# Optimization experiments

Measured on AMD Instinct MI355X. Metric: run time of the kernel, lower is better.

## Reference

```python
import jax, jax.numpy as jnp
import numpy as np

B, N, K, D = 8, 4096, 16, 256


def layer_norm(x, g, b, eps=1e-5):
    m = jnp.mean(x, axis=-1, keepdims=True)
    v = jnp.var(x, axis=-1, keepdims=True)
    return (x - m) * jax.lax.rsqrt(v + eps) * g + b


def setup_inputs() -> dict:
    key = jax.random.key(0)
    ks = jax.random.split(key, 8)

    def lin(k, fi, fo):
        return (jax.random.normal(k, (fi, fo), jnp.float32) / np.sqrt(fi).astype(np.float32),
                jnp.zeros((fo,), jnp.float32))

    coordinates = jax.random.normal(ks[0], (B, N, 3), jnp.float32)
    W1, b1 = lin(ks[1], 10, D // 4)
    W2, b2 = lin(ks[2], D // 4, D // 2)
    W3, b3 = lin(ks[3], D // 2, D)
    Wa1, ba1 = lin(ks[4], D, D)
    Wa2, ba2 = lin(ks[5], D, D)
    return {
        'coordinates': coordinates,
        'W1': W1, 'b1': b1, 'g1': jnp.ones((D // 4,)), 'be1': jnp.zeros((D // 4,)),
        'W2': W2, 'b2': b2, 'g2': jnp.ones((D // 2,)), 'be2': jnp.zeros((D // 2,)),
        'W3': W3, 'b3': b3, 'g3': jnp.ones((D,)), 'be3': jnp.zeros((D,)),
        'Wa1': Wa1, 'ba1': ba1, 'ga1': jnp.ones((D,)), 'bea1': jnp.zeros((D,)),
        'Wa2': Wa2, 'ba2': ba2,
    }


def reference(coordinates, W1, b1, g1, be1, W2, b2, g2, be2, W3, b3, g3, be3,
              Wa1, ba1, ga1, bea1, Wa2, ba2):
    # kNN via squared-distance matrix (monotone in Euclidean distance)
    sq = jnp.sum(coordinates * coordinates, axis=-1)  # [B,N]
    d2 = sq[:, :, None] + sq[:, None, :] - 2.0 * jnp.einsum('bnd,bmd->bnm', coordinates, coordinates)
    _, idx = jax.lax.top_k(-d2, K)  # smallest K distances, [B,N,K]

    nbr = jax.vmap(lambda c, i: c[i])(coordinates, idx)  # [B,N,K,3]
    rel = nbr - coordinates[:, :, None, :]               # relative positions
    dist = jnp.linalg.norm(rel, axis=-1, keepdims=True)  # [B,N,K,1]
    rn = rel / (dist + 1e-6)
    axy = jnp.arctan2(rn[..., 1], rn[..., 0])[..., None]
    axz = jnp.arctan2(rn[..., 2], rn[..., 0])[..., None]
    ayz = jnp.arctan2(rn[..., 2], rn[..., 1])[..., None]
    geom = jnp.concatenate([dist, rel, axy, axz, ayz, rn], axis=-1)  # [B,N,K,10]

    # encoder MLP
    h = jax.nn.relu(layer_norm(geom @ W1 + b1, g1, be1))
    h = jax.nn.relu(layer_norm(h @ W2 + b2, g2, be2))
    h = layer_norm(h @ W3 + b3, g3, be3)

    agg = jnp.mean(h, axis=2)  # mean over neighbors -> [B,N,D]

    # aggregator MLP
    out = jax.nn.relu(layer_norm(agg @ Wa1 + ba1, ga1, bea1)) @ Wa2 + ba2
    return out
```

## Files before the change

kernel.cpp:

```cpp
#include <hip/hip_runtime.h>
#include <hip/hip_bf16.h>
#include <math.h>

#define BB 8
#define NN 4096
#define KK 16
#define DD 256

typedef __hip_bfloat16 bf16;
typedef _Float16 half8 __attribute__((ext_vector_type(8)));
typedef float f32x4 __attribute__((ext_vector_type(4)));

union HFU { _Float16 h; unsigned short u; };
__device__ __forceinline__ unsigned short f2h(float x) { HFU v; v.h = (_Float16)x; return v.u; }

#define CONV_TOTAL 273344
#define O_COORD 0
#define O_W1 98304
#define O_b1 98944
#define O_g1 99008
#define O_be1 99072
#define O_W2 99136
#define O_b2 107328
#define O_g2 107456
#define O_be2 107584
#define O_W3 107712
#define O_b3 140480
#define O_g3 140736
#define O_be3 140992
#define O_Wa1 141248
#define O_ba1 206784
#define O_ga1 207040
#define O_bea1 207296
#define O_Wa2 207552
#define O_ba2 273088

#define F_W1 0
#define F_W2 2048
#define F_W3 10240
#define F_A1 43008
#define F_A2 108544
#define FRAG_TOTAL 174080

struct SrcPtrs {
  const void* p[19];
};

__global__ __launch_bounds__(256) void convert_kernel(SrcPtrs sp, float* __restrict__ dst) {
  static constexpr int OFF[20] = {
      0,      98304,  98944,  99008,  99072,  99136,  107328, 107456, 107584,
      107712, 140480, 140736, 140992, 141248, 206784, 207040, 207296, 207552,
      273088, 273344};
  const int i = blockIdx.x * 256 + threadIdx.x;
  if (i >= CONV_TOTAL) return;
  const unsigned tag = ((const unsigned*)sp.p[3])[0];
  const bool isb = (tag == 0x3F803F80u);
  int s = 0;
#pragma unroll
  for (int j = 1; j < 19; j++)
    if (i >= OFF[j]) s = j;
  const int local = i - OFF[s];
  float v = isb ? __bfloat162float(((const bf16*)sp.p[s])[local])
                : ((const float*)sp.p[s])[local];
  dst[i] = v;
}

__global__ __launch_bounds__(256) void swizzle_kernel(const float* __restrict__ conv,
                                                      unsigned short* __restrict__ frag) {
  const int t = blockIdx.x * 256 + threadIdx.x;
  if (t >= FRAG_TOTAL) return;
  int l, e;
  if (t < 2048) { l = 0; e = t; }
  else if (t < 10240) { l = 1; e = t - 2048; }
  else if (t < 43008) { l = 2; e = t - 10240; }
  else if (t < 108544) { l = 3; e = t - 43008; }
  else { l = 4; e = t - 108544; }
  static constexpr int WOFF[5] = {O_W1, O_W2, O_W3, O_Wa1, O_Wa2};
  static constexpr int NDIM[5] = {64, 128, 256, 256, 256};
  static constexpr int NTC[5] = {4, 8, 16, 16, 16};
  static constexpr int KREAL[5] = {10, 64, 128, 256, 256};
  static constexpr int HOFF[5] = {F_W1, F_W2, F_W3, F_A1, F_A2};
  const int j = e & 7;
  const int lane = (e >> 3) & 63;
  const int tile = e >> 9;
  const int nt = tile % NTC[l];
  const int kt = tile / NTC[l];
  const int k = kt * 32 + (lane >> 4) * 8 + j;
  const int n = nt * 16 + (lane & 15);
  float w = (k < KREAL[l]) ? conv[WOFF[l] + k * NDIM[l] + n] : 0.0f;
  frag[HOFF[l] + e] = f2h(w);
}

__device__ __forceinline__ float sq3_rn(float x, float y, float z) {
  return __fadd_rn(__fadd_rn(__fmul_rn(x, x), __fmul_rn(y, y)), __fmul_rn(z, z));
}
__device__ __forceinline__ float dot3_rn(float ax, float ay, float az, float bx, float by, float bz) {
  return __fadd_rn(__fadd_rn(__fmul_rn(ax, bx), __fmul_rn(ay, by)), __fmul_rn(az, bz));
}
__device__ __forceinline__ unsigned f2ord(float f) {
  unsigned u = __float_as_uint(f);
  return (u & 0x80000000u) ? ~u : (u | 0x80000000u);
}
__device__ __forceinline__ float ord2f(unsigned o) {
  unsigned u = (o & 0x80000000u) ? (o & 0x7FFFFFFFu) : ~o;
  return __uint_as_float(u);
}

__device__ __forceinline__ unsigned long long bitonic64(unsigned long long key, int lane) {
#pragma unroll
  for (int k = 2; k <= 64; k <<= 1) {
#pragma unroll
    for (int jj = k >> 1; jj > 0; jj >>= 1) {
      unsigned long long v = __shfl_xor(key, jj, 64);
      bool asc = ((lane & k) == 0);
      bool up = ((lane & jj) != 0);
      unsigned long long mn = (key < v) ? key : v;
      unsigned long long mx2 = (key < v) ? v : key;
      key = (up == asc) ? mx2 : mn;
    }
  }
  return key;
}

__global__ __launch_bounds__(512) void cellsort_kernel(const float* __restrict__ conv,
                                                       float4* __restrict__ sorted,
                                                       int* __restrict__ sidx) {
  __shared__ unsigned hist[512];
  __shared__ unsigned scanb[512];
  const int b = blockIdx.x;
  const int tid = threadIdx.x;
  const float* cb = conv + O_COORD + (size_t)b * NN * 3;
  hist[tid] = 0;
  __syncthreads();
  float xs[8], ys[8], zs[8];
  int cell[8];
  unsigned rank[8];
#pragma unroll
  for (int u = 0; u < 8; u++) {
    int p = u * 512 + tid;
    float x = cb[p * 3 + 0], y = cb[p * 3 + 1], z = cb[p * 3 + 2];
    xs[u] = x; ys[u] = y; zs[u] = z;
    int ix = min(7, max(0, (int)floorf(x + 4.0f)));
    int iy = min(7, max(0, (int)floorf(y + 4.0f)));
    int iz = min(7, max(0, (int)floorf(z + 4.0f)));
    int m = ((ix & 1) | ((ix & 2) << 2) | ((ix & 4) << 4)) |
            (((iy & 1) | ((iy & 2) << 2) | ((iy & 4) << 4)) << 1) |
            (((iz & 1) | ((iz & 2) << 2) | ((iz & 4) << 4)) << 2);
    cell[u] = m;
    rank[u] = atomicAdd(&hist[m], 1u);
  }
  __syncthreads();
  scanb[tid] = hist[tid];
  __syncthreads();
  for (int off = 1; off < 512; off <<= 1) {
    unsigned t = (tid >= off) ? scanb[tid - off] : 0u;
    __syncthreads();
    scanb[tid] += t;
    __syncthreads();
  }
#pragma unroll
  for (int u = 0; u < 8; u++) {
    unsigned base = scanb[cell[u]] - hist[cell[u]];
    unsigned pos = base + rank[u];
    sorted[(size_t)b * NN + pos] =
        make_float4(xs[u], ys[u], zs[u], sq3_rn(xs[u], ys[u], zs[u]));
    sidx[(size_t)b * NN + pos] = u * 512 + tid;
  }
}

__global__ __launch_bounds__(256) void knn_wave_kernel(const float4* __restrict__ soa,
                                                       const int* __restrict__ sI,
                                                       int* __restrict__ idx_out) {
  const int lane = threadIdx.x & 63;
  const int wid = blockIdx.x * 4 + (threadIdx.x >> 6);
  const int q0 = wid * 4;
  const int b = q0 >> 12;
  const float4* P = soa + (size_t)b * NN;
  const int* I = sI + (size_t)b * NN;
  const int qr = q0 & (NN - 1);
  const int base = qr >> 6;

  float cx[4], cy[4], cz[4], sqn[4];
  int qix[4];
#pragma unroll
  for (int j = 0; j < 4; j++) {
    float4 c = P[qr + j];
    cx[j] = c.x; cy[j] = c.y; cz[j] = c.z; sqn[j] = c.w;
    qix[j] = I[qr + j];
  }

  unsigned long long R[4], pend[4];
  float tauf[4];
  int A[4] = {0, 0, 0, 0};
#pragma unroll
  for (int j = 0; j < 4; j++) pend[j] = ~0ull;

  auto MERGE = [&](int j) {
    unsigned long long key =
        (lane < 16) ? R[j] : ((lane < 16 + A[j]) ? pend[j] : ~0ull);
    key = bitonic64(key, lane);
    R[j] = key;
    tauf[j] = ord2f((unsigned)(unsigned long long)__builtin_amdgcn_readlane(
        (int)(unsigned)(key >> 32), 15));
    A[j] = 0;
  };

  auto APPEND = [&](int j, unsigned long long msk, int cc, unsigned long long key) {
    unsigned rank = __builtin_amdgcn_mbcnt_hi(
        (unsigned)(msk >> 32), __builtin_amdgcn_mbcnt_lo((unsigned)msk, 0u));
    const bool flag = ((msk >> lane) & 1ull) != 0;
    const int lim = 16 + A[j];
    const int nf = lane - (int)rank;
    const int dst = flag ? (lim + (int)rank) : (nf < lim ? nf : nf + cc);
    int src = __builtin_amdgcn_ds_permute(dst << 2, lane) & 63;
    unsigned lo = (unsigned)__builtin_amdgcn_ds_bpermute(src << 2, (int)(unsigned)key);
    unsigned hi = (unsigned)__builtin_amdgcn_ds_bpermute(src << 2, (int)(unsigned)(key >> 32));
    const bool cons = (lane >= lim) && (lane < lim + cc);
    if (cons) pend[j] = (((unsigned long long)hi) << 32) | lo;
    A[j] += cc;
  };

  const int b0 = base * 64 + lane;
  float4 f0 = P[b0];
  int i0 = I[b0];
  const int b1 = ((base + 1) & 63) * 64 + lane;
  float4 f1 = P[b1];
  int i1 = I[b1];
  const int b2i = ((base + 2) & 63) * 64 + lane;
  float4 f2 = P[b2i];
  int i2 = I[b2i];

#pragma unroll
  for (int j = 0; j < 4; j++) {
    float dot = dot3_rn(cx[j], cy[j], cz[j], f0.x, f0.y, f0.z);
    float d2 = __fsub_rn(__fadd_rn(sqn[j], f0.w), __fmul_rn(2.0f, dot));
    unsigned long long key =
        (((unsigned long long)f2ord(d2)) << 32) | (unsigned)i0;
    key = bitonic64(key, lane);
    R[j] = key;
    tauf[j] = ord2f((unsigned)(unsigned long long)__builtin_amdgcn_readlane(
        (int)(unsigned)(key >> 32), 15));
  }

  for (int t = 1; t < 64; t++) {
    const float4 c = f1;
    const int iv = i1;
    f1 = f2; i1 = i2;
    if (t + 2 < 64) {
      const int nb = ((base + t + 2) & 63) * 64 + lane;
      f2 = P[nb];
      i2 = I[nb];
    }
    float d2v[4];
    unsigned long long pm[4];
#pragma unroll
    for (int j = 0; j < 4; j++) {
      float dot = dot3_rn(cx[j], cy[j], cz[j], c.x, c.y, c.z);
      d2v[j] = __fsub_rn(__fadd_rn(sqn[j], c.w), __fmul_rn(2.0f, dot));
      pm[j] = __ballot(d2v[j] <= tauf[j]);
    }
    if (!(pm[0] | pm[1] | pm[2] | pm[3])) continue;
#pragma unroll
    for (int j = 0; j < 4; j++) {
      unsigned long long rem = pm[j];
      if (!rem) continue;
      const unsigned long long key =
          (((unsigned long long)f2ord(d2v[j])) << 32) | (unsigned)iv;
      int cc = __builtin_popcountll(rem);
      while (A[j] + cc > 48) {
        if (A[j] == 0) {
          unsigned long long take = rem & 0xFFFFFFFFull;
          APPEND(j, take, __builtin_popcountll(take), key);
          rem ^= take;
        }
        MERGE(j);
        rem &= __ballot(d2v[j] <= tauf[j]);
        cc = __builtin_popcountll(rem);
      }
      if (cc) APPEND(j, rem, cc, key);
    }
  }

#pragma unroll
  for (int j = 0; j < 4; j++) {
    if (A[j]) MERGE(j);
    if (lane < KK)
      idx_out[((size_t)b * NN + (unsigned)qix[j]) * KK + lane] =
          (int)(R[j] & 0xFFFFFFFFull);
  }
}

template <int KT>
__device__ __forceinline__ void load_afrags(half8* A, const unsigned short* lF,
                                            int rowe, int lane) {
#pragma unroll
  for (int kt = 0; kt < KT; kt++) {
    int off = (lane & 15) * rowe + kt * 32 + (lane >> 4) * 8;
    A[kt] = *reinterpret_cast<const half8*>(lF + off);
  }
}

template <int NT>
__device__ __forceinline__ void init_acc(f32x4* acc, const float* __restrict__ bias,
                                         int lane) {
  const int col = lane & 15;
#pragma unroll
  for (int nt = 0; nt < NT; nt++) {
    float bv = bias[nt * 16 + col];
    acc[nt] = {bv, bv, bv, bv};
  }
}

template <int KT, int NT>
__device__ __forceinline__ void gemm_acc(f32x4* acc, const half8* A,
                                         const unsigned short* bb, int lane) {
#pragma unroll
  for (int kt = 0; kt < KT; kt++)
#pragma unroll
    for (int nt = 0; nt < NT; nt++) {
      const half8 bf = *reinterpret_cast<const half8*>(bb + (kt * NT + nt) * 512 + lane * 8);
      acc[nt] = __builtin_amdgcn_mfma_f32_16x16x32_f16(A[kt], bf, acc[nt], 0, 0, 0);
    }
}

template <int NT>
__device__ __forceinline__ void ln_stats(const f32x4* acc, float* m, float* rs) {
  float s[4] = {0.f, 0.f, 0.f, 0.f}, s2[4] = {0.f, 0.f, 0.f, 0.f};
#pragma unroll
  for (int nt = 0; nt < NT; nt++)
#pragma unroll
    for (int r = 0; r < 4; r++) {
      float v = acc[nt][r];
      s[r] += v;
      s2[r] += v * v;
    }
#pragma unroll
  for (int msk = 1; msk <= 8; msk <<= 1)
#pragma unroll
    for (int r = 0; r < 4; r++) {
      s[r] += __shfl_xor(s[r], msk, 64);
      s2[r] += __shfl_xor(s2[r], msk, 64);
    }
  const float invN = 1.0f / (NT * 16);
#pragma unroll
  for (int r = 0; r < 4; r++) {
    m[r] = s[r] * invN;
    float var = s2[r] * invN - m[r] * m[r];
    rs[r] = rsqrtf(var + 1e-5f);
  }
}

template <int NT, bool RELU>
__device__ __forceinline__ void ln_store(const f32x4* acc, const float* m, const float* rs,
                                         const float* __restrict__ g, const float* __restrict__ be,
                                         unsigned short* lF, int rowe, int lane) {
  const int col = lane & 15;
  const int rbase = (lane >> 4) * 4;
#pragma unroll
  for (int nt = 0; nt < NT; nt++) {
    float gv = g[nt * 16 + col], bv = be[nt * 16 + col];
#pragma unroll
    for (int r = 0; r < 4; r++) {
      float v = (acc[nt][r] - m[r]) * rs[r] * gv + bv;
      if (RELU) v = fmaxf(v, 0.0f);
      lF[(rbase + r) * rowe + nt * 16 + col] = f2h(v);
    }
  }
}

__device__ __forceinline__ void stage_b(unsigned short* bbuf,
                                        const unsigned short* __restrict__ src,
                                        int n_u4, int tid) {
  const uint4* s = reinterpret_cast<const uint4*>(src);
  uint4* d = reinterpret_cast<uint4*>(bbuf);
  for (int i = tid; i < n_u4; i += 256) d[i] = s[i];
}

#define ROWE_E 136
#define PSTR_E (16 * ROWE_E)

__global__ __launch_bounds__(256, 3) void encoder_mfma(
    const float* __restrict__ conv, const int* __restrict__ nbr,
    const unsigned short* __restrict__ frag, unsigned short* __restrict__ agF) {
  __shared__ unsigned short planes[4 * PSTR_E];
  __shared__ unsigned short Bbuf[10240];
  const int tid = threadIdx.x;
  const int lane = tid & 63;
  const int wave = tid >> 6;
  const int point = blockIdx.x * 4 + wave;
  const int b = point >> 12;
  const int n = point & (NN - 1);
  const float* cb = conv + O_COORD + (size_t)b * NN * 3;
  unsigned short* lF = planes + wave * PSTR_E;
  const int g = lane >> 4;
  const int col = lane & 15;

  {
    int pl = tid >> 6, row = (tid >> 2) & 15, part = tid & 3;
    *reinterpret_cast<uint4*>(planes + pl * PSTR_E + row * ROWE_E + part * 8) =
        make_uint4(0u, 0u, 0u, 0u);
    stage_b(Bbuf, frag + F_W1, 1280, tid);
  }
  __syncthreads();

  if (lane < 16) {
    float cxq = cb[n * 3 + 0], cyq = cb[n * 3 + 1], czq = cb[n * 3 + 2];
    int id = nbr[(size_t)point * KK + lane];
    float rx = __fsub_rn(cb[id * 3 + 0], cxq);
    float ry = __fsub_rn(cb[id * 3 + 1], cyq);
    float rz = __fsub_rn(cb[id * 3 + 2], czq);
    float dist = __fsqrt_rn(sq3_rn(rx, ry, rz));
    float den = __fadd_rn(dist, 1e-6f);
    float ux = __fdiv_rn(rx, den), uy = __fdiv_rn(ry, den), uz = __fdiv_rn(rz, den);
    float ge[10];
    ge[0] = dist; ge[1] = rx; ge[2] = ry; ge[3] = rz;
    ge[4] = atan2f(uy, ux); ge[5] = atan2f(uz, ux); ge[6] = atan2f(uz, uy);
    ge[7] = ux; ge[8] = uy; ge[9] = uz;
#pragma unroll
    for (int c = 0; c < 10; c++) lF[lane * ROWE_E + c] = f2h(ge[c]);
  }

  {
    half8 x0;
    load_afrags<1>(&x0, lF, ROWE_E, lane);
    f32x4 a1[4];
#pragma unroll
    for (int m = 0; m < 4; m++) {
      const float4 bv = *reinterpret_cast<const float4*>(conv + O_b1 + m * 16 + g * 4);
      a1[m] = {bv.x, bv.y, bv.z, bv.w};
      const half8 wf = *reinterpret_cast<const half8*>(Bbuf + m * 512 + lane * 8);
      a1[m] = __builtin_amdgcn_mfma_f32_16x16x32_f16(wf, x0, a1[m], 0, 0, 0);
    }
    float s = 0.f, s2 = 0.f;
#pragma unroll
    for (int m = 0; m < 4; m++)
#pragma unroll
      for (int r = 0; r < 4; r++) { float v = a1[m][r]; s += v; s2 += v * v; }
    s += __shfl_xor(s, 16, 64); s += __shfl_xor(s, 32, 64);
    s2 += __shfl_xor(s2, 16, 64); s2 += __shfl_xor(s2, 32, 64);
    const float mu = s * (1.0f / 64.0f);
    const float rsg = rsqrtf(s2 * (1.0f / 64.0f) - mu * mu + 1e-5f);
#pragma unroll
    for (int m = 0; m < 4; m++) {
      const float4 gv = *reinterpret_cast<const float4*>(conv + O_g1 + m * 16 + g * 4);
      const float4 bev = *reinterpret_cast<const float4*>(conv + O_be1 + m * 16 + g * 4);
      unsigned long long pk = 0;
#pragma unroll
      for (int r = 0; r < 4; r++) {
        float v = fmaxf((a1[m][r] - mu) * rsg * (&gv.x)[r] + (&bev.x)[r], 0.0f);
        pk |= ((unsigned long long)f2h(v)) << (16 * r);
      }
      *reinterpret_cast<unsigned long long*>(lF + col * ROWE_E + m * 16 + g * 4) = pk;
    }
  }

  {
    half8 x2[2];
    load_afrags<2>(x2, lF, ROWE_E, lane);
    f32x4 a2[8];
#pragma unroll
    for (int m = 0; m < 8; m++) {
      const float4 bv = *reinterpret_cast<const float4*>(conv + O_b2 + m * 16 + g * 4);
      a2[m] = {bv.x, bv.y, bv.z, bv.w};
    }
#pragma unroll
    for (int kt = 0; kt < 2; kt++)
#pragma unroll
      for (int m = 0; m < 8; m++) {
        const half8 wf =
            *reinterpret_cast<const half8*>(Bbuf + 2048 + (kt * 8 + m) * 512 + lane * 8);
        a2[m] = __builtin_amdgcn_mfma_f32_16x16x32_f16(wf, x2[kt], a2[m], 0, 0, 0);
      }
    float s = 0.f, s2 = 0.f;
#pragma unroll
    for (int m = 0; m < 8; m++)
#pragma unroll
      for (int r = 0; r < 4; r++) { float v = a2[m][r]; s += v; s2 += v * v; }
    s += __shfl_xor(s, 16, 64); s += __shfl_xor(s, 32, 64);
    s2 += __shfl_xor(s2, 16, 64); s2 += __shfl_xor(s2, 32, 64);
    const float mu = s * (1.0f / 128.0f);
    const float rsg = rsqrtf(s2 * (1.0f / 128.0f) - mu * mu + 1e-5f);
#pragma unroll
    for (int m = 0; m < 8; m++) {
      const float4 gv = *reinterpret_cast<const float4*>(conv + O_g2 + m * 16 + g * 4);
      const float4 bev = *reinterpret_cast<const float4*>(conv + O_be2 + m * 16 + g * 4);
      unsigned long long pk = 0;
#pragma unroll
      for (int r = 0; r < 4; r++) {
        float v = fmaxf((a2[m][r] - mu) * rsg * (&gv.x)[r] + (&bev.x)[r], 0.0f);
        pk |= ((unsigned long long)f2h(v)) << (16 * r);
      }
      *reinterpret_cast<unsigned long long*>(lF + col * ROWE_E + m * 16 + g * 4) = pk;
    }
  }

  half8 A3[4];
  load_afrags<4>(A3, lF, ROWE_E, lane);
  f32x4 acc[16];
  init_acc<16>(acc, conv + O_b3, lane);
  {
    const unsigned short* W3 = frag + F_W3;
#pragma unroll
    for (int kt = 0; kt < 4; kt++)
#pragma unroll
      for (int nt = 0; nt < 16; nt++) {
        const half8 bf =
            *reinterpret_cast<const half8*>(W3 + (kt * 16 + nt) * 512 + lane * 8);
        acc[nt] = __builtin_amdgcn_mfma_f32_16x16x32_f16(A3[kt], bf, acc[nt], 0, 0, 0);
      }
  }

  {
    float m[4], rs[4];
    ln_stats<16>(acc, m, rs);
    float sv[16];
#pragma unroll
    for (int nt = 0; nt < 16; nt++) {
      float gvv = conv[O_g3 + nt * 16 + col], bvv = conv[O_be3 + nt * 16 + col];
      float s = 0.f;
#pragma unroll
      for (int r = 0; r < 4; r++) s += (acc[nt][r] - m[r]) * rs[r] * gvv + bvv;
      s += __shfl_xor(s, 16, 64);
      s += __shfl_xor(s, 32, 64);
      sv[nt] = s * (1.0f / 16.0f);
    }
    if (lane < 16) {
      size_t base = (size_t)point * DD;
#pragma unroll
      for (int nt = 0; nt < 16; nt++) agF[base + nt * 16 + lane] = f2h(sv[nt]);
    }
  }
}

#define ROWE_A 264

__global__ __launch_bounds__(256) void aggmlp_mfma(
    const float* __restrict__ conv, const unsigned short* __restrict__ agF,
    const unsigned short* __restrict__ a1, const unsigned short* __restrict__ a2,
    const unsigned* __restrict__ g1raw, void* __restrict__ out) {
  __shared__ unsigned short lds[4][16 * ROWE_A];
  const int lane = threadIdx.x & 63;
  const int wave = threadIdx.x >> 6;
  const int row0 = (blockIdx.x * 4 + wave) * 16;
  unsigned short* lF = lds[wave];

#pragma unroll
  for (int t = 0; t < 8; t++) {
    int v = t * 64 + lane;
    int row = v >> 5;
    int c0 = (v & 31) * 8;
    *reinterpret_cast<uint4*>(lF + row * ROWE_A + c0) =
        *reinterpret_cast<const uint4*>(agF + ((size_t)(row0 + row) * DD + c0));
  }
  __syncthreads();

  float m[4], rs[4];
  f32x4 acc[16];
  {
    half8 A[8];
    load_afrags<8>(A, lF, ROWE_A, lane);
    init_acc<16>(acc, conv + O_ba1, lane);
    gemm_acc<8, 16>(acc, A, a1, lane);
    ln_stats<16>(acc, m, rs);
    ln_store<16, true>(acc, m, rs, conv + O_ga1, conv + O_bea1, lF, ROWE_A, lane);
  }
  __syncthreads();
  {
    half8 A[8];
    load_afrags<8>(A, lF, ROWE_A, lane);
    init_acc<16>(acc, conv + O_ba2, lane);
    gemm_acc<8, 16>(acc, A, a2, lane);
  }
  const bool isb = (g1raw[0] == 0x3F803F80u);
  const int col = lane & 15;
  const int rbase = (lane >> 4) * 4;
  if (isb) {
    bf16* o = (bf16*)out;
#pragma unroll
    for (int nt = 0; nt < 16; nt++)
#pragma unroll
      for (int r = 0; r < 4; r++)
        o[(size_t)(row0 + rbase + r) * DD + nt * 16 + col] = __float2bfloat16(acc[nt][r]);
  } else {
    float* o = (float*)out;
#pragma unroll
    for (int nt = 0; nt < 16; nt++)
#pragma unroll
      for (int r = 0; r < 4; r++)
        o[(size_t)(row0 + rbase + r) * DD + nt * 16 + col] = acc[nt][r];
  }
}

extern "C" void kernel_launch(void* const* d_in, const int* in_sizes, int n_in,
                              void* d_out, int out_size, void* d_ws, size_t ws_size,
                              hipStream_t stream) {
  char* ws = (char*)d_ws;
  float* conv = (float*)ws;
  int* idx_ws = (int*)(ws + 1093376);
  unsigned short* agF = (unsigned short*)(ws + 3190528);
  unsigned short* frag = (unsigned short*)(ws + 19967744);
  float4* sorted = (float4*)(ws + 20315904);
  int* sidx = (int*)(ws + 20840192);

  SrcPtrs sp;
  for (int i = 0; i < 19; i++) sp.p[i] = d_in[i];

  convert_kernel<<<(CONV_TOTAL + 255) / 256, 256, 0, stream>>>(sp, conv);
  swizzle_kernel<<<(FRAG_TOTAL + 255) / 256, 256, 0, stream>>>(conv, frag);
  cellsort_kernel<<<BB, 512, 0, stream>>>(conv, sorted, sidx);

  knn_wave_kernel<<<BB * NN / 16, 256, 0, stream>>>(sorted, sidx, idx_ws);

  encoder_mfma<<<BB * NN / 4, 256, 0, stream>>>(conv, idx_ws, frag, agF);

  aggmlp_mfma<<<BB * NN / 64, 256, 0, stream>>>(conv, agF, frag + F_A1, frag + F_A2,
                                                (const unsigned*)d_in[3], d_out);
}
```

Baseline: 384.5 us.

## Prune kNN candidate blocks using per-block bounding boxes

Adds a kernel that computes an axis-aligned bounding box for each 64-point block of cell-sorted coordinates. The kNN kernel then computes a lower-bound distance from its 4 queries to each block and visits only blocks whose bound is within the current worst top-K threshold plus a margin, rechecking the bound as the threshold tightens. This is meant to skip most of the 64-block brute-force scan per wave. It adds a small extra launch and a data-dependent loop with irregular loads. The margin is a safety fudge, and pruning with squared distances from fp32-rounded keys could in rare cases drop true neighbors.

```diff
diff --git a/kernel.cpp b/kernel.cpp
--- a/kernel.cpp
+++ b/kernel.cpp
@@ -41,6 +41,8 @@
 #define F_A1 43008
 #define F_A2 108544
 #define FRAG_TOTAL 174080
+
+#define PRUNE_MARGIN 0.0625f
 
 struct SrcPtrs {
   const void* p[19];
@@ -168,8 +170,33 @@
   }
 }
 
+__global__ __launch_bounds__(256) void bbox_kernel(const float4* __restrict__ sorted,
+                                                   float4* __restrict__ bbmn,
+                                                   float4* __restrict__ bbmx) {
+  const int lane = threadIdx.x & 63;
+  const int gid = blockIdx.x * 4 + (threadIdx.x >> 6);
+  float4 p = sorted[(size_t)gid * 64 + lane];
+  float mnx = p.x, mny = p.y, mnz = p.z;
+  float mxx = p.x, mxy = p.y, mxz = p.z;
+#pragma unroll
+  for (int d = 1; d < 64; d <<= 1) {
+    mnx = fminf(mnx, __shfl_xor(mnx, d, 64));
+    mny = fminf(mny, __shfl_xor(mny, d, 64));
+    mnz = fminf(mnz, __shfl_xor(mnz, d, 64));
+    mxx = fmaxf(mxx, __shfl_xor(mxx, d, 64));
+    mxy = fmaxf(mxy, __shfl_xor(mxy, d, 64));
+    mxz = fmaxf(mxz, __shfl_xor(mxz, d, 64));
+  }
+  if (lane == 0) {
+    bbmn[gid] = make_float4(mnx, mny, mnz, 0.0f);
+    bbmx[gid] = make_float4(mxx, mxy, mxz, 0.0f);
+  }
+}
+
 __global__ __launch_bounds__(256) void knn_wave_kernel(const float4* __restrict__ soa,
                                                        const int* __restrict__ sI,
+                                                       const float4* __restrict__ bbmn,
+                                                       const float4* __restrict__ bbmx,
                                                        int* __restrict__ idx_out) {
   const int lane = threadIdx.x & 63;
   const int wid = blockIdx.x * 4 + (threadIdx.x >> 6);
@@ -188,6 +215,23 @@
     cx[j] = c.x; cy[j] = c.y; cz[j] = c.z; sqn[j] = c.w;
     qix[j] = I[qr + j];
   }
+
+  float4 bmn = bbmn[b * 64 + lane];
+  float4 bmx = bbmx[b * 64 + lane];
+  float4 f0 = P[base * 64 + lane];
+  int i0 = I[base * 64 + lane];
+
+  float qnx = fminf(fminf(cx[0], cx[1]), fminf(cx[2], cx[3]));
+  float qxx = fmaxf(fmaxf(cx[0], cx[1]), fmaxf(cx[2], cx[3]));
+  float qny = fminf(fminf(cy[0], cy[1]), fminf(cy[2], cy[3]));
+  float qxy = fmaxf(fmaxf(cy[0], cy[1]), fmaxf(cy[2], cy[3]));
+  float qnz = fminf(fminf(cz[0], cz[1]), fminf(cz[2], cz[3]));
+  float qxz = fmaxf(fmaxf(cz[0], cz[1]), fmaxf(cz[2], cz[3]));
+
+  float dx = fmaxf(fmaxf(bmn.x - qxx, qnx - bmx.x), 0.0f);
+  float dy = fmaxf(fmaxf(bmn.y - qxy, qny - bmx.y), 0.0f);
+  float dz = fmaxf(fmaxf(bmn.z - qxz, qnz - bmx.z), 0.0f);
+  const float lb = dx * dx + dy * dy + dz * dz;
 
   unsigned long long R[4], pend[4];
   float tauf[4];
@@ -220,16 +264,6 @@
     A[j] += cc;
   };
 
-  const int b0 = base * 64 + lane;
-  float4 f0 = P[b0];
-  int i0 = I[b0];
-  const int b1 = ((base + 1) & 63) * 64 + lane;
-  float4 f1 = P[b1];
-  int i1 = I[b1];
-  const int b2i = ((base + 2) & 63) * 64 + lane;
-  float4 f2 = P[b2i];
-  int i2 = I[b2i];
-
 #pragma unroll
   for (int j = 0; j < 4; j++) {
     float dot = dot3_rn(cx[j], cy[j], cz[j], f0.x, f0.y, f0.z);
@@ -242,14 +276,34 @@
         (int)(unsigned)(key >> 32), 15));
   }
 
-  for (int t = 1; t < 64; t++) {
-    const float4 c = f1;
-    const int iv = i1;
-    f1 = f2; i1 = i2;
-    if (t + 2 < 64) {
-      const int nb = ((base + t + 2) & 63) * 64 + lane;
-      f2 = P[nb];
-      i2 = I[nb];
+  float tmax = fmaxf(fmaxf(tauf[0], tauf[1]), fmaxf(tauf[2], tauf[3]));
+  unsigned long long mask =
+      __ballot(lb <= tmax + PRUNE_MARGIN) & ~(1ull << base);
+  const int ro = (base + 1) & 63;
+  auto rot = [&](unsigned long long m) {
+    return ro ? ((m >> ro) | (m << (64 - ro))) : m;
+  };
+  unsigned long long rm = rot(mask);
+
+  int tA = -1, tB = -1, iA = 0, iB = 0;
+  float4 fA, fB;
+  if (rm) {
+    int tz = __builtin_ctzll(rm); rm &= rm - 1;
+    tA = (ro + tz) & 63; fA = P[tA * 64 + lane]; iA = I[tA * 64 + lane];
+  }
+  if (rm) {
+    int tz = __builtin_ctzll(rm); rm &= rm - 1;
+    tB = (ro + tz) & 63; fB = P[tB * 64 + lane]; iB = I[tB * 64 + lane];
+  }
+  while (tA >= 0) {
+    const float4 c = fA;
+    const int iv = iA;
+    tA = tB; fA = fB; iA = iB;
+    if (rm) {
+      int tz = __builtin_ctzll(rm); rm &= rm - 1;
+      tB = (ro + tz) & 63; fB = P[tB * 64 + lane]; iB = I[tB * 64 + lane];
+    } else {
+      tB = -1;
     }
     float d2v[4];
     unsigned long long pm[4];
@@ -279,6 +333,8 @@
       }
       if (cc) APPEND(j, rem, cc, key);
     }
+    tmax = fmaxf(fmaxf(tauf[0], tauf[1]), fmaxf(tauf[2], tauf[3]));
+    rm &= rot(__ballot(lb <= tmax + PRUNE_MARGIN));
   }
 
 #pragma unroll
@@ -601,6 +657,8 @@
   unsigned short* frag = (unsigned short*)(ws + 19967744);
   float4* sorted = (float4*)(ws + 20315904);
   int* sidx = (int*)(ws + 20840192);
+  float4* bbmn = (float4*)(ws + 20971264);
+  float4* bbmx = (float4*)(ws + 20979456);
 
   SrcPtrs sp;
   for (int i = 0; i < 19; i++) sp.p[i] = d_in[i];
@@ -608,8 +666,9 @@
   convert_kernel<<<(CONV_TOTAL + 255) / 256, 256, 0, stream>>>(sp, conv);
   swizzle_kernel<<<(FRAG_TOTAL + 255) / 256, 256, 0, stream>>>(conv, frag);
   cellsort_kernel<<<BB, 512, 0, stream>>>(conv, sorted, sidx);
-
-  knn_wave_kernel<<<BB * NN / 16, 256, 0, stream>>>(sorted, sidx, idx_ws);
+  bbox_kernel<<<BB * 64 / 4, 256, 0, stream>>>(sorted, bbmn, bbmx);
+
+  knn_wave_kernel<<<BB * NN / 16, 256, 0, stream>>>(sorted, sidx, bbmn, bbmx, idx_ws);
 
   encoder_mfma<<<BB * NN / 4, 256, 0, stream>>>(conv, idx_ws, frag, agF);
 
```

Result: faster. 375.7 us (median of 2 runs) (-2.3%).
